# Optimization experiments

Hardware: AMD Instinct MI355X
Metric: run time of the kernel (lower is better)

## Reference

```python
import jax, jax.numpy as jnp
import numpy as np

B, H, W, C, NH, WS = 4, 128, 128, 128, 4, 8
N = WS * WS
HD = C // NH
SCALE = HD ** -0.5
MLP_H = 4 * C


def _rel_index():
    coords = np.stack(np.meshgrid(np.arange(WS), np.arange(WS), indexing='ij'))
    flat = coords.reshape(2, -1)
    rel = (flat[:, :, None] - flat[:, None, :]).transpose(1, 2, 0).astype(np.int64)
    rel[..., 0] += WS - 1
    rel[..., 1] += WS - 1
    rel[..., 0] *= 2 * WS - 1
    return jnp.asarray(rel.sum(-1))  # (N, N)

REL_IDX = _rel_index()


def layer_norm(x, w, b):
    m = jnp.mean(x, -1, keepdims=True)
    v = jnp.mean((x - m) ** 2, -1, keepdims=True)
    return (x - m) * jax.lax.rsqrt(v + 1e-5) * w + b


def window_partition(x):  # (B, H*W, C) -> (B*nW, N, C)
    t = x.reshape(B, H // WS, WS, W // WS, WS, C).transpose(0, 1, 3, 2, 4, 5)
    return t.reshape(-1, N, C)


def window_reverse(wins):  # (B*nW, N, C) -> (B, H*W, C)
    t = wins.reshape(B, H // WS, W // WS, WS, WS, C).transpose(0, 1, 3, 2, 4, 5)
    return t.reshape(B, H * W, C)


def setup_inputs():
    key = jax.random.key(0)
    ks = jax.random.split(key, 8)
    rn = lambda k, s: jax.random.normal(k, s, jnp.float32) * 0.02
    return {
        'x': jax.random.normal(ks[0], (B, H * W, C), jnp.float32),
        'd': jax.random.normal(ks[1], (B, H * W, C), jnp.float32),
        'rpb_table': rn(ks[2], ((2 * WS - 1) ** 2, NH)),
        'norm1_w': jnp.ones((C,), jnp.float32), 'norm1_b': jnp.zeros((C,), jnp.float32),
        'norm2_w': jnp.ones((C,), jnp.float32), 'norm2_b': jnp.zeros((C,), jnp.float32),
        'qkv1_w': rn(ks[3], (4 * C, C)), 'qkv1_b': jnp.zeros((4 * C,), jnp.float32),
        'proj_w': rn(ks[4], (C, C)), 'proj_b': jnp.zeros((C,), jnp.float32),
        'fc1_w': rn(ks[5], (MLP_H, C)), 'fc1_b': jnp.zeros((MLP_H,), jnp.float32),
        'fc2_w': rn(ks[6], (C, MLP_H)), 'fc2_b': jnp.zeros((C,), jnp.float32),
    }


def _attn_core(xw, dw, rpb_table, qkv1_w, qkv1_b, proj_w, proj_b):
    def qkv(t):
        q = (t @ qkv1_w.T + qkv1_b).reshape(-1, N, 4, NH, HD)
        return jnp.moveaxis(q, 2, 0).transpose(0, 1, 3, 2, 4)  # (4, B_, NH, N, HD)

    q_r, k_r, v_r, q_rd = qkv(xw)
    q_d, k_d, v_d, q_dr = qkv(dw)
    bias = rpb_table[REL_IDX].transpose(2, 0, 1)  # (NH, N, N)
    sm = jax.nn.softmax
    dot = lambda q, k: jnp.einsum('bhnd,bhmd->bhnm', q * SCALE, k)
    attn = sm(dot(q_r, k_r) + bias[None])      # bias only on r-branch (as in torch)
    attn_rd = sm(dot(q_dr, k_r))
    attn_d = sm(dot(q_d, k_d))
    attn_dr = sm(dot(q_rd, k_d))
    av = lambda a, v: jnp.einsum('bhnm,bhmd->bhnd', a, v).transpose(0, 2, 1, 3).reshape(-1, N, C)
    x_out = av(attn, v_r) + av(attn_rd, v_r)
    d_out = av(attn_dr, v_d) + av(attn_d, v_d)
    return x_out @ proj_w.T + proj_b, d_out @ proj_w.T + proj_b


def reference(x, d, rpb_table, norm1_w, norm1_b, norm2_w, norm2_b, qkv1_w, qkv1_b, proj_w, proj_b, fc1_w, fc1_b, fc2_w, fc2_b):
    xw = window_partition(layer_norm(x, norm1_w, norm1_b))
    dw = window_partition(layer_norm(d, norm1_w, norm1_b))
    xa, da = _attn_core(xw, dw, rpb_table, qkv1_w, qkv1_b, proj_w, proj_b)
    x = x + window_reverse(xa)
    d = d + window_reverse(da)
    mlp = lambda t: jax.nn.gelu(t @ fc1_w.T + fc1_b, approximate=False) @ fc2_w.T + fc2_b
    x = x + mlp(layer_norm(x, norm2_w, norm2_b))
    d = d + mlp(layer_norm(d, norm2_w, norm2_b))
    return x, d
```

## Files before the change

kernel.cpp:

```cpp
#include <hip/hip_runtime.h>
#include <hip/hip_bf16.h>
#include <math.h>

typedef short bf16x8 __attribute__((ext_vector_type(8)));
typedef float f32x4 __attribute__((ext_vector_type(4)));

#define QKSCALE_L2E 0.25505402227437564f
#define LOG2E 1.4426950408889634f

__device__ __forceinline__ unsigned short f2bf(float f) {
  __hip_bfloat16 h = __float2bfloat16(f);
  return *reinterpret_cast<unsigned short*>(&h);
}
__device__ __forceinline__ float bf2f(unsigned short h) {
  return __uint_as_float(((unsigned int)h) << 16);
}
__device__ __forceinline__ unsigned int pk2(float lo, float hi) {
  __hip_bfloat162 h = __float22bfloat162_rn(make_float2(lo, hi));
  return *reinterpret_cast<unsigned int*>(&h);
}
__device__ __forceinline__ bf16x8 pack8(const float* g) {
  union { unsigned int u[4]; bf16x8 v; } t;
  t.u[0] = pk2(g[0], g[1]); t.u[1] = pk2(g[2], g[3]);
  t.u[2] = pk2(g[4], g[5]); t.u[3] = pk2(g[6], g[7]);
  return t.v;
}

__device__ __forceinline__ bf16x8 ldsv(const unsigned short* base, int row, int strideHalfs, int kHalf, int swzMask) {
  int byte = row * strideHalfs * 2 + kHalf * 2;
  byte ^= (row & swzMask) << 4;
  return *(const bf16x8*)((const char*)base + byte);
}
__device__ __forceinline__ void ldss(unsigned short* base, int row, int strideHalfs, int col, int swzMask, unsigned short v) {
  int byte = row * strideHalfs * 2 + col * 2;
  byte ^= (row & swzMask) << 4;
  *(unsigned short*)((char*)base + byte) = v;
}
__device__ __forceinline__ void ldst64(unsigned short* base, int row, int strideHalfs, int colHalf, int swzMask, unsigned int lo, unsigned int hi) {
  int byte = row * strideHalfs * 2 + colHalf * 2;
  byte ^= (row & swzMask) << 4;
  uint2 val; val.x = lo; val.y = hi;
  *(uint2*)((char*)base + byte) = val;
}
__device__ __forceinline__ void ldst32q(unsigned short* base, int row, int colHalf, unsigned int v) {
  int byte = row * 64 + colHalf * 2;
  byte ^= ((row >> 2) & 1) << 6;
  *(unsigned int*)((char*)base + byte) = v;
}
__device__ __forceinline__ bf16x8 ldsvq(const unsigned short* base, int row, int kHalf) {
  int byte = row * 64 + kHalf * 2;
  byte ^= ((row >> 2) & 1) << 6;
  return *(const bf16x8*)((const char*)base + byte);
}

__global__ void prep_kernel(
    const float* __restrict__ qkv1_w, const float* __restrict__ qkv1_b,
    const float* __restrict__ proj_w, const float* __restrict__ fc1_w,
    const float* __restrict__ fc2_w,  const float* __restrict__ rpb,
    unsigned short* __restrict__ Wqkvf, unsigned short* __restrict__ Wprojf,
    unsigned short* __restrict__ Wfc1f, unsigned short* __restrict__ Wfc2f,
    float* __restrict__ bqkv, float* __restrict__ biasmat)
{
  int i = blockIdx.x * 256 + threadIdx.x;
  if (i < 65536) {
    int j = i & 7, lane = (i >> 3) & 63, kk = (i >> 9) & 3;
    int sub16 = (i >> 11) & 1, h = (i >> 12) & 3, comp = i >> 14;
    int row = comp * 128 + h * 32 + sub16 * 16 + (lane & 15);
    int col = kk * 32 + (lane >> 4) * 8 + j;
    float sc = (comp == 0 || comp == 3) ? QKSCALE_L2E : 1.f;
    Wqkvf[i] = f2bf(qkv1_w[row * 128 + col] * sc);
  }
  int o = i - 65536;
  if (o >= 0 && o < 16384) {
    int j = o & 7, lane = (o >> 3) & 63, kk = (o >> 9) & 3, nf = o >> 11;
    int row = nf * 16 + (lane & 15);
    int cp = kk * 32 + (lane >> 4) * 8 + j;
    int H = cp >> 5, q = cp & 31, a = q >> 1, b = q & 1;
    Wprojf[o] = f2bf(proj_w[row * 128 + H * 32 + 16 * b + a]);
  }
  o -= 16384;
  if (o >= 0 && o < 65536) {
    int j = o & 7, lane = (o >> 3) & 63, kk = (o >> 9) & 3, n16 = o >> 11;
    int row = n16 * 16 + (lane & 15);
    int cp = kk * 32 + (lane >> 4) * 8 + j;
    Wfc1f[o] = f2bf(fc1_w[row * 128 + 16 * (cp & 7) + (cp >> 3)]);
  }
  o -= 65536;
  if (o >= 0 && o < 65536) {
    int j = o & 7, lane = (o >> 3) & 63, kk = (o >> 9) & 15, n8 = o >> 13;
    int row = n8 * 16 + (lane & 15);
    int m = kk * 32 + (lane >> 4) * 8 + j;
    int src = (m >> 6) * 64 + 16 * (m & 3) + ((m >> 2) & 15);
    Wfc2f[o] = f2bf(fc2_w[row * 512 + src]);
  }
  o -= 65536;
  if (o >= 0 && o < 512) {
    int comp = o >> 7;
    bqkv[o] = qkv1_b[o] * ((comp == 0 || comp == 3) ? QKSCALE_L2E : 1.f);
  }
  o -= 512;
  if (o >= 0 && o < 16384) {
    int hh = o >> 12, n = (o >> 6) & 63, m = o & 63;
    int di = (n >> 3) - (m >> 3) + 7, dj = (n & 7) - (m & 7) + 7;
    biasmat[o] = rpb[(di * 15 + dj) * 4 + hh] * LOG2E;
  }
}

__global__ void __launch_bounds__(256) ln1_kernel(
    const float* __restrict__ x_in, const float* __restrict__ d_in_,
    const float* __restrict__ n1w, const float* __restrict__ n1b,
    unsigned short* __restrict__ xg)
{
  const int s = blockIdx.x >> 10;
  const int row0 = (blockIdx.x & 1023) * 64;
  const int t = threadIdx.x >> 2, q4 = threadIdx.x & 3;
  const int grow = row0 + t;
  const int b2 = grow >> 14, rem = grow & 16383;
  const int gy = rem >> 7, gx = rem & 127;
  const int win = b2 * 256 + (gy >> 3) * 16 + (gx >> 3);
  const int tok = (gy & 7) * 8 + (gx & 7);
  const float* src = (s ? d_in_ : x_in) + (size_t)grow * 128 + q4 * 32;
  float v[32];
  float sum = 0.f, ss = 0.f;
#pragma unroll
  for (int i = 0; i < 8; ++i) {
    float4 f = ((const float4*)src)[i];
    v[i * 4 + 0] = f.x; v[i * 4 + 1] = f.y; v[i * 4 + 2] = f.z; v[i * 4 + 3] = f.w;
    sum += f.x + f.y + f.z + f.w;
    ss += f.x * f.x + f.y * f.y + f.z * f.z + f.w * f.w;
  }
  sum += __shfl_xor(sum, 1); sum += __shfl_xor(sum, 2);
  ss  += __shfl_xor(ss, 1);  ss  += __shfl_xor(ss, 2);
  float mean = sum * (1.f / 128.f);
  float var = ss * (1.f / 128.f) - mean * mean;
  float rs = rsqrtf(var + 1e-5f);
  unsigned short* base = xg + ((size_t)(s * 1024 + win)) * 8192
                         + ((tok >> 4) * 4 + q4) * 512 + (tok & 15) * 8;
#pragma unroll
  for (int i = 0; i < 4; ++i) {
    float g[8];
#pragma unroll
    for (int jj = 0; jj < 8; ++jj) {
      int c = q4 * 32 + i * 8 + jj;
      g[jj] = (v[i * 8 + jj] - mean) * rs * n1w[c] + n1b[c];
    }
    *(bf16x8*)(base + i * 128) = pack8(g);
  }
}

__global__ void __launch_bounds__(256, 4) attn_kernel(
    const unsigned short* __restrict__ xg,
    const unsigned short* __restrict__ Wqkvf, const float* __restrict__ bqkv,
    const float* __restrict__ biasmat,
    unsigned short* __restrict__ aout)
{
  __shared__ unsigned short smem[2][10240];

  const int tid = threadIdx.x, wid = tid >> 6, lane = tid & 63;
  const int l4 = lane >> 4, l15 = lane & 15;
  const int win = blockIdx.x & 1023, h = blockIdx.x >> 10;
  const f32x4 fzero = {0.f, 0.f, 0.f, 0.f};

  bf16x8 aF[2][4];
#pragma unroll
  for (int s = 0; s < 2; ++s) {
    const unsigned short* xw = xg + ((size_t)(s * 1024 + win)) * 8192;
#pragma unroll
    for (int kk = 0; kk < 4; ++kk)
      aF[s][kk] = *(const bf16x8*)(xw + (wid * 4 + kk) * 512 + lane * 8);
  }

  {
    f32x4 acc[2][8];
#pragma unroll
    for (int s = 0; s < 2; ++s)
#pragma unroll
      for (int n = 0; n < 8; ++n) acc[s][n] = fzero;
#pragma unroll
    for (int kk = 0; kk < 4; ++kk)
#pragma unroll
      for (int nf = 0; nf < 8; ++nf) {
        const int frag = (((nf >> 1) * 4 + h) * 2 + (nf & 1)) * 4 + kk;
        bf16x8 bb = *(const bf16x8*)(Wqkvf + frag * 512 + lane * 8);
        acc[0][nf] = __builtin_amdgcn_mfma_f32_16x16x32_bf16(aF[0][kk], bb, acc[0][nf], 0, 0, 0);
        acc[1][nf] = __builtin_amdgcn_mfma_f32_16x16x32_bf16(aF[1][kk], bb, acc[1][nf], 0, 0, 0);
      }
    float bv[8];
#pragma unroll
    for (int nf = 0; nf < 8; ++nf) bv[nf] = bqkv[(nf >> 1) * 128 + h * 32 + (nf & 1) * 16 + l15];
#pragma unroll
    for (int s = 0; s < 2; ++s)
#pragma unroll
      for (int r = 0; r < 4; ++r) {
        const int tw = wid * 16 + l4 * 4 + r;
        ldst32q(smem[s] + 0,    tw, 2 * l15, pk2(acc[s][0][r] + bv[0], acc[s][1][r] + bv[1]));
        ldst32q(smem[s] + 4096, tw, 2 * l15, pk2(acc[s][2][r] + bv[2], acc[s][3][r] + bv[3]));
        ldst32q(smem[s] + 2048, tw, 2 * l15, pk2(acc[s][6][r] + bv[6], acc[s][7][r] + bv[7]));
        const int vc = 16 * l4 + 4 * r + wid;
        ldss(smem[s] + 8192, l15,      64, vc, 7, f2bf(acc[s][4][r] + bv[4]));
        ldss(smem[s] + 8192, 16 + l15, 64, vc, 7, f2bf(acc[s][5][r] + bv[5]));
      }
  }
  __syncthreads();

  const int s = wid >> 1, kind = wid & 1;
  bf16x8 aR[4], kR[4];
  {
    const unsigned short* Ab = kind ? (smem[1 - s] + 2048) : (smem[s] + 0);
    const unsigned short* Kb = smem[s] + 4096;
#pragma unroll
    for (int mf = 0; mf < 4; ++mf) aR[mf] = ldsvq(Ab, mf * 16 + l15, l4 * 8);
#pragma unroll
    for (int nf = 0; nf < 4; ++nf) kR[nf] = ldsvq(Kb, nf * 16 + l15, l4 * 8);
  }

  f32x4 sc[4][4];
#pragma unroll
  for (int mf = 0; mf < 4; ++mf)
#pragma unroll
    for (int nf = 0; nf < 4; ++nf) sc[mf][nf] = fzero;
#pragma unroll
  for (int mf = 0; mf < 4; ++mf)
#pragma unroll
    for (int nf = 0; nf < 4; ++nf)
      sc[mf][nf] = __builtin_amdgcn_mfma_f32_16x16x32_bf16(aR[mf], kR[nf], sc[mf][nf], 0, 0, 0);

  if (s == 0 && kind == 0) {
#pragma unroll
    for (int mf = 0; mf < 4; ++mf)
#pragma unroll
      for (int nf = 0; nf < 4; ++nf)
#pragma unroll
        for (int r = 0; r < 4; ++r) {
          int row = mf * 16 + l4 * 4 + r, col = nf * 16 + l15;
          sc[mf][nf][r] += biasmat[(h * 64 + row) * 64 + col];
        }
  }
#pragma unroll
  for (int mf = 0; mf < 4; ++mf) {
    float M = sc[mf][0][0];
#pragma unroll
    for (int nf = 0; nf < 4; ++nf)
#pragma unroll
      for (int r = 0; r < 4; ++r) M = fmaxf(M, sc[mf][nf][r]);
    M = fmaxf(M, __shfl_xor(M, 1));
    M = fmaxf(M, __shfl_xor(M, 2));
    M = fmaxf(M, __shfl_xor(M, 4));
    M = fmaxf(M, __shfl_xor(M, 8));
#pragma unroll
    for (int r = 0; r < 4; ++r) {
      float e0 = __builtin_amdgcn_exp2f(sc[mf][0][r] - M);
      float e1 = __builtin_amdgcn_exp2f(sc[mf][1][r] - M);
      float e2 = __builtin_amdgcn_exp2f(sc[mf][2][r] - M);
      float e3 = __builtin_amdgcn_exp2f(sc[mf][3][r] - M);
      float sm = e0 + e1 + e2 + e3;
      sm += __shfl_xor(sm, 1); sm += __shfl_xor(sm, 2);
      sm += __shfl_xor(sm, 4); sm += __shfl_xor(sm, 8);
      float inv = __builtin_amdgcn_rcpf(sm);
      sc[mf][0][r] = e0 * inv; sc[mf][1][r] = e1 * inv;
      sc[mf][2][r] = e2 * inv; sc[mf][3][r] = e3 * inv;
    }
  }
  __syncthreads();
  {
    unsigned short* Ptgt = smem[s] + (kind ? 4096 : 0);
#pragma unroll
    for (int mf = 0; mf < 4; ++mf)
#pragma unroll
      for (int r = 0; r < 4; ++r)
        ldst64(Ptgt, mf * 16 + l4 * 4 + r, 64, 4 * l15, 7,
               pk2(sc[mf][0][r], sc[mf][1][r]), pk2(sc[mf][2][r], sc[mf][3][r]));
  }
  __syncthreads();

  {
    const unsigned short* Vt = smem[s] + 8192;
    bf16x8 vR[2][2];
#pragma unroll
    for (int kk = 0; kk < 2; ++kk)
#pragma unroll
      for (int nf = 0; nf < 2; ++nf) vR[kk][nf] = ldsv(Vt, nf * 16 + l15, 64, kk * 32 + l4 * 8, 7);
    f32x4 pv[2][2];
    pv[0][0] = fzero; pv[0][1] = fzero; pv[1][0] = fzero; pv[1][1] = fzero;
#pragma unroll
    for (int pb_i = 0; pb_i < 2; ++pb_i) {
      const unsigned short* Pbuf = smem[s] + pb_i * 4096;
#pragma unroll
      for (int kk = 0; kk < 2; ++kk) {
        bf16x8 pa0 = ldsv(Pbuf, kind * 32 + l15, 64, kk * 32 + l4 * 8, 7);
        bf16x8 pa1 = ldsv(Pbuf, kind * 32 + 16 + l15, 64, kk * 32 + l4 * 8, 7);
#pragma unroll
        for (int nf = 0; nf < 2; ++nf) {
          pv[0][nf] = __builtin_amdgcn_mfma_f32_16x16x32_bf16(pa0, vR[kk][nf], pv[0][nf], 0, 0, 0);
          pv[1][nf] = __builtin_amdgcn_mfma_f32_16x16x32_bf16(pa1, vR[kk][nf], pv[1][nf], 0, 0, 0);
        }
      }
    }
#pragma unroll
    for (int mf = 0; mf < 2; ++mf)
#pragma unroll
      for (int r = 0; r < 4; ++r) {
        int tw = kind * 32 + mf * 16 + l4 * 4 + r;
        *(unsigned int*)(aout + ((size_t)s * 65536 + (size_t)win * 64 + tw) * 128 + h * 32 + 2 * l15) =
            pk2(pv[mf][0][r], pv[mf][1][r]);
      }
  }
}

__global__ void __launch_bounds__(256, 4) proj_kernel(
    const unsigned short* __restrict__ aout, const unsigned short* __restrict__ Wprojf,
    const float* __restrict__ projb,
    const float* __restrict__ x_in, const float* __restrict__ d_in_,
    const float* __restrict__ n2w, const float* __restrict__ n2b,
    unsigned short* __restrict__ xv, unsigned short* __restrict__ xn2)
{
  const int tid = threadIdx.x, wid = tid >> 6, lane = tid & 63;
  const int l4 = lane >> 4, l15 = lane & 15;
  const int s = blockIdx.x >> 9, blk = blockIdx.x & 511;
  const int row0 = blk * 128 + wid * 32;
  const unsigned short* A = aout + (size_t)s * 65536 * 128;
  const f32x4 fzero = {0.f, 0.f, 0.f, 0.f};

  bf16x8 aF[2][4];
#pragma unroll
  for (int mf = 0; mf < 2; ++mf)
#pragma unroll
    for (int kk = 0; kk < 4; ++kk)
      aF[mf][kk] = *(const bf16x8*)(A + (size_t)(row0 + mf * 16 + l15) * 128 + kk * 32 + l4 * 8);

  f32x4 acc[2][8];
#pragma unroll
  for (int mf = 0; mf < 2; ++mf)
#pragma unroll
    for (int nf = 0; nf < 8; ++nf) acc[mf][nf] = fzero;
#pragma unroll
  for (int kk = 0; kk < 4; ++kk)
#pragma unroll
    for (int nf = 0; nf < 8; ++nf) {
      bf16x8 bb = *(const bf16x8*)(Wprojf + (nf * 4 + kk) * 512 + lane * 8);
      acc[0][nf] = __builtin_amdgcn_mfma_f32_16x16x32_bf16(aF[0][kk], bb, acc[0][nf], 0, 0, 0);
      acc[1][nf] = __builtin_amdgcn_mfma_f32_16x16x32_bf16(aF[1][kk], bb, acc[1][nf], 0, 0, 0);
    }

  float pbv[8], w2v[8], b2v[8];
#pragma unroll
  for (int nf = 0; nf < 8; ++nf) {
    int col = nf * 16 + l15;
    pbv[nf] = projb[col]; w2v[nf] = n2w[col]; b2v[nf] = n2b[col];
  }
  const float* resid = s ? d_in_ : x_in;
#pragma unroll
  for (int mf = 0; mf < 2; ++mf)
#pragma unroll
    for (int r = 0; r < 4; ++r) {
      int t = row0 + mf * 16 + l4 * 4 + r;
      int w2 = t >> 6, tk = t & 63;
      int b2 = w2 >> 8, hb = (w2 >> 4) & 15, wb = w2 & 15;
      int grow = b2 * 16384 + hb * 1024 + (tk >> 3) * 128 + wb * 8 + (tk & 7);
      float v[8];
      float sum = 0.f, ssq = 0.f;
#pragma unroll
      for (int nf = 0; nf < 8; ++nf) {
        size_t off = (size_t)grow * 128 + nf * 16 + l15;
        float val = acc[mf][nf][r] + pbv[nf] + resid[off];
        v[nf] = val; sum += val; ssq += val * val;
      }
#pragma unroll
      for (int nf = 0; nf < 8; ++nf)
        xv[((size_t)s * 65536 + grow) * 128 + nf * 16 + l15] = f2bf(v[nf]);
      sum += __shfl_xor(sum, 1); sum += __shfl_xor(sum, 2);
      sum += __shfl_xor(sum, 4); sum += __shfl_xor(sum, 8);
      ssq += __shfl_xor(ssq, 1); ssq += __shfl_xor(ssq, 2);
      ssq += __shfl_xor(ssq, 4); ssq += __shfl_xor(ssq, 8);
      float mean = sum * (1.f / 128.f);
      float var = ssq * (1.f / 128.f) - mean * mean;
      float rs = rsqrtf(var + 1e-5f);
      float g[8];
#pragma unroll
      for (int nf = 0; nf < 8; ++nf) g[nf] = (v[nf] - mean) * rs * w2v[nf] + b2v[nf];
      size_t fidx = ((size_t)s * 4096 + (grow >> 4)) * 4 + (l15 >> 2);
      *(bf16x8*)(xn2 + fidx * 512 + ((l15 & 3) * 16 + (grow & 15)) * 8) = pack8(g);
    }
}

__global__ void __launch_bounds__(512, 2) mlp_kernel(
    const unsigned short* __restrict__ xn2, const unsigned short* __restrict__ xv,
    const unsigned short* __restrict__ Wfc1f, const float* __restrict__ fc1b,
    const unsigned short* __restrict__ Wfc2f, const float* __restrict__ fc2b,
    float* __restrict__ out)
{
  __shared__ unsigned short hbuf[32 * 512];
  const int tid = threadIdx.x, wid = tid >> 6, lane = tid & 63;
  const int l4 = lane >> 4, l15 = lane & 15;
  const f32x4 fzero = {0.f, 0.f, 0.f, 0.f};

  bf16x8 wf1[16], wf2[16];
#pragma unroll
  for (int q = 0; q < 16; ++q)
    wf1[q] = *(const bf16x8*)(Wfc1f + (size_t)((wid * 4 + (q >> 2)) * 4 + (q & 3)) * 512 + lane * 8);
#pragma unroll
  for (int kk = 0; kk < 16; ++kk)
    wf2[kk] = *(const bf16x8*)(Wfc2f + (size_t)(wid * 16 + kk) * 512 + lane * 8);

  float b1v[4];
#pragma unroll
  for (int nf = 0; nf < 4; ++nf) b1v[nf] = fc1b[wid * 64 + nf * 16 + l15];
  const float b2c = fc2b[wid * 16 + l15];
  const int ocol = wid * 16 + l15;

  const size_t tokbase = (size_t)blockIdx.x * 256;

  for (int it = 0; it < 8; ++it) {
    if (it) __syncthreads();
    const size_t tb = tokbase + it * 32;
    f32x4 acc[2][4];
#pragma unroll
    for (int mf = 0; mf < 2; ++mf)
#pragma unroll
      for (int nf = 0; nf < 4; ++nf) acc[mf][nf] = fzero;
#pragma unroll
    for (int mf = 0; mf < 2; ++mf)
#pragma unroll
      for (int kk = 0; kk < 4; ++kk) {
        bf16x8 a = *(const bf16x8*)(xn2 + (((tb >> 4) + mf) * 4 + kk) * 512 + lane * 8);
#pragma unroll
        for (int nf = 0; nf < 4; ++nf)
          acc[mf][nf] = __builtin_amdgcn_mfma_f32_16x16x32_bf16(a, wf1[nf * 4 + kk], acc[mf][nf], 0, 0, 0);
      }
#pragma unroll
    for (int mf = 0; mf < 2; ++mf)
#pragma unroll
      for (int r = 0; r < 4; ++r) {
        float g[4];
#pragma unroll
        for (int nf = 0; nf < 4; ++nf) {
          float vv = acc[mf][nf][r] + b1v[nf];
          float x2 = vv * vv;
          float u2 = vv * fmaf(-0.10294455f, x2, -2.3022078f);
          float e = __builtin_amdgcn_exp2f(u2);
          g[nf] = vv * __builtin_amdgcn_rcpf(1.f + e);
        }
        ldst64(hbuf, mf * 16 + l4 * 4 + r, 512, wid * 64 + l15 * 4, 7,
               pk2(g[0], g[1]), pk2(g[2], g[3]));
      }
    __syncthreads();
    f32x4 a2[2];
    a2[0] = fzero; a2[1] = fzero;
#pragma unroll
    for (int kk = 0; kk < 16; ++kk) {
      bf16x8 h0 = ldsv(hbuf, l15, 512, kk * 32 + l4 * 8, 7);
      bf16x8 h1 = ldsv(hbuf, 16 + l15, 512, kk * 32 + l4 * 8, 7);
      a2[0] = __builtin_amdgcn_mfma_f32_16x16x32_bf16(h0, wf2[kk], a2[0], 0, 0, 0);
      a2[1] = __builtin_amdgcn_mfma_f32_16x16x32_bf16(h1, wf2[kk], a2[1], 0, 0, 0);
    }
#pragma unroll
    for (int mf = 0; mf < 2; ++mf)
#pragma unroll
      for (int r = 0; r < 4; ++r) {
        int row = mf * 16 + l4 * 4 + r;
        size_t off = (tb + row) * 128 + ocol;
        float res = bf2f(xv[off]);
        out[off] = a2[mf][r] + b2c + res;
      }
  }
}

extern "C" void kernel_launch(void* const* d_in, const int* in_sizes, int n_in,
                              void* d_out, int out_size, void* d_ws, size_t ws_size,
                              hipStream_t stream) {
  const float* x    = (const float*)d_in[0];
  const float* dd   = (const float*)d_in[1];
  const float* rpb  = (const float*)d_in[2];
  const float* n1w  = (const float*)d_in[3];
  const float* n1b  = (const float*)d_in[4];
  const float* n2w  = (const float*)d_in[5];
  const float* n2b  = (const float*)d_in[6];
  const float* qkvw = (const float*)d_in[7];
  const float* qkvb = (const float*)d_in[8];
  const float* pw   = (const float*)d_in[9];
  const float* pb   = (const float*)d_in[10];
  const float* f1w  = (const float*)d_in[11];
  const float* f1b  = (const float*)d_in[12];
  const float* f2w  = (const float*)d_in[13];
  const float* f2b  = (const float*)d_in[14];
  float* out = (float*)d_out;
  char* ws = (char*)d_ws;
  unsigned short* Wqkvf  = (unsigned short*)(ws);
  unsigned short* Wprojf = (unsigned short*)(ws + 131072);
  unsigned short* Wfc1f  = (unsigned short*)(ws + 163840);
  unsigned short* Wfc2f  = (unsigned short*)(ws + 294912);
  float* bqkv            = (float*)(ws + 425984);
  float* biasmat         = (float*)(ws + 428032);
  unsigned short* aout   = (unsigned short*)(ws + 524288);
  unsigned short* xn2    = (unsigned short*)(ws + 524288 + 33554432);
  unsigned short* xv     = (unsigned short*)(ws + 524288 + 67108864);
  unsigned short* xg     = (unsigned short*)d_out;

  prep_kernel<<<dim3(899), dim3(256), 0, stream>>>(qkvw, qkvb, pw, f1w, f2w, rpb,
                                                   Wqkvf, Wprojf, Wfc1f, Wfc2f, bqkv, biasmat);
  ln1_kernel<<<dim3(2048), dim3(256), 0, stream>>>(x, dd, n1w, n1b, xg);
  attn_kernel<<<dim3(4096), dim3(256), 0, stream>>>(xg, Wqkvf, bqkv, biasmat, aout);
  proj_kernel<<<dim3(1024), dim3(256), 0, stream>>>(aout, Wprojf, pb, x, dd, n2w, n2b, xv, xn2);
  mlp_kernel<<<dim3(512), dim3(512), 0, stream>>>(xn2, xv, Wfc1f, f1b, Wfc2f, f2b, out);
}
```

Baseline: 203.6 us.

## Split attention blocks per stream, recomputing cross-query to halve shared memory

The attention kernel now launches one block per (window, head, stream) instead of one per (window, head) covering both streams. Each block projects Q, K and V for its own stream and recomputes the cross-query projection from the other stream's input. This halves shared memory and per-wave work, so more blocks can be resident (the launch bounds go from 4 to 8). In exchange it adds redundant loads of the other stream's input and redundant weight fetches per block.

```diff
diff --git a/kernel.cpp b/kernel.cpp
--- a/kernel.cpp
+++ b/kernel.cpp
@@ -148,96 +148,94 @@
   }
 }
 
-__global__ void __launch_bounds__(256, 4) attn_kernel(
+__global__ void __launch_bounds__(256, 8) attn_kernel(
     const unsigned short* __restrict__ xg,
     const unsigned short* __restrict__ Wqkvf, const float* __restrict__ bqkv,
     const float* __restrict__ biasmat,
     unsigned short* __restrict__ aout)
 {
-  __shared__ unsigned short smem[2][10240];
+  __shared__ unsigned short smem[10240];
 
   const int tid = threadIdx.x, wid = tid >> 6, lane = tid & 63;
   const int l4 = lane >> 4, l15 = lane & 15;
-  const int win = blockIdx.x & 1023, h = blockIdx.x >> 10;
+  const int win = blockIdx.x & 1023;
+  const int p = blockIdx.x >> 10;
+  const int h = p & 3, s = p >> 2;
   const f32x4 fzero = {0.f, 0.f, 0.f, 0.f};
 
-  bf16x8 aF[2][4];
-#pragma unroll
-  for (int s = 0; s < 2; ++s) {
-    const unsigned short* xw = xg + ((size_t)(s * 1024 + win)) * 8192;
-#pragma unroll
-    for (int kk = 0; kk < 4; ++kk)
-      aF[s][kk] = *(const bf16x8*)(xw + (wid * 4 + kk) * 512 + lane * 8);
-  }
-
+  bf16x8 aFs[4], aFo[4];
   {
-    f32x4 acc[2][8];
-#pragma unroll
-    for (int s = 0; s < 2; ++s)
-#pragma unroll
-      for (int n = 0; n < 8; ++n) acc[s][n] = fzero;
+    const unsigned short* xws = xg + ((size_t)(s * 1024 + win)) * 8192;
+    const unsigned short* xwo = xg + ((size_t)((1 - s) * 1024 + win)) * 8192;
+#pragma unroll
+    for (int kk = 0; kk < 4; ++kk) {
+      aFs[kk] = *(const bf16x8*)(xws + (wid * 4 + kk) * 512 + lane * 8);
+      aFo[kk] = *(const bf16x8*)(xwo + (wid * 4 + kk) * 512 + lane * 8);
+    }
+  }
+
+  {
+    f32x4 acc[8];
+#pragma unroll
+    for (int n = 0; n < 8; ++n) acc[n] = fzero;
 #pragma unroll
     for (int kk = 0; kk < 4; ++kk)
 #pragma unroll
       for (int nf = 0; nf < 8; ++nf) {
         const int frag = (((nf >> 1) * 4 + h) * 2 + (nf & 1)) * 4 + kk;
         bf16x8 bb = *(const bf16x8*)(Wqkvf + frag * 512 + lane * 8);
-        acc[0][nf] = __builtin_amdgcn_mfma_f32_16x16x32_bf16(aF[0][kk], bb, acc[0][nf], 0, 0, 0);
-        acc[1][nf] = __builtin_amdgcn_mfma_f32_16x16x32_bf16(aF[1][kk], bb, acc[1][nf], 0, 0, 0);
+        acc[nf] = __builtin_amdgcn_mfma_f32_16x16x32_bf16(nf < 6 ? aFs[kk] : aFo[kk], bb, acc[nf], 0, 0, 0);
       }
     float bv[8];
 #pragma unroll
     for (int nf = 0; nf < 8; ++nf) bv[nf] = bqkv[(nf >> 1) * 128 + h * 32 + (nf & 1) * 16 + l15];
 #pragma unroll
-    for (int s = 0; s < 2; ++s)
-#pragma unroll
-      for (int r = 0; r < 4; ++r) {
-        const int tw = wid * 16 + l4 * 4 + r;
-        ldst32q(smem[s] + 0,    tw, 2 * l15, pk2(acc[s][0][r] + bv[0], acc[s][1][r] + bv[1]));
-        ldst32q(smem[s] + 4096, tw, 2 * l15, pk2(acc[s][2][r] + bv[2], acc[s][3][r] + bv[3]));
-        ldst32q(smem[s] + 2048, tw, 2 * l15, pk2(acc[s][6][r] + bv[6], acc[s][7][r] + bv[7]));
-        const int vc = 16 * l4 + 4 * r + wid;
-        ldss(smem[s] + 8192, l15,      64, vc, 7, f2bf(acc[s][4][r] + bv[4]));
-        ldss(smem[s] + 8192, 16 + l15, 64, vc, 7, f2bf(acc[s][5][r] + bv[5]));
-      }
+    for (int r = 0; r < 4; ++r) {
+      const int tw = wid * 16 + l4 * 4 + r;
+      ldst32q(smem + 0,    tw, 2 * l15, pk2(acc[0][r] + bv[0], acc[1][r] + bv[1]));
+      ldst32q(smem + 4096, tw, 2 * l15, pk2(acc[2][r] + bv[2], acc[3][r] + bv[3]));
+      ldst32q(smem + 2048, tw, 2 * l15, pk2(acc[6][r] + bv[6], acc[7][r] + bv[7]));
+      const int vc = 16 * l4 + 4 * r + wid;
+      ldss(smem + 8192, l15,      64, vc, 7, f2bf(acc[4][r] + bv[4]));
+      ldss(smem + 8192, 16 + l15, 64, vc, 7, f2bf(acc[5][r] + bv[5]));
+    }
   }
   __syncthreads();
 
-  const int s = wid >> 1, kind = wid & 1;
-  bf16x8 aR[4], kR[4];
+  const int kind = wid & 1, rh = wid >> 1;
+  bf16x8 aR[2], kR[4];
   {
-    const unsigned short* Ab = kind ? (smem[1 - s] + 2048) : (smem[s] + 0);
-    const unsigned short* Kb = smem[s] + 4096;
-#pragma unroll
-    for (int mf = 0; mf < 4; ++mf) aR[mf] = ldsvq(Ab, mf * 16 + l15, l4 * 8);
-#pragma unroll
-    for (int nf = 0; nf < 4; ++nf) kR[nf] = ldsvq(Kb, nf * 16 + l15, l4 * 8);
-  }
-
-  f32x4 sc[4][4];
-#pragma unroll
-  for (int mf = 0; mf < 4; ++mf)
+    const unsigned short* Ab = kind ? (smem + 2048) : (smem + 0);
+#pragma unroll
+    for (int mf = 0; mf < 2; ++mf) aR[mf] = ldsvq(Ab, rh * 32 + mf * 16 + l15, l4 * 8);
+#pragma unroll
+    for (int nf = 0; nf < 4; ++nf) kR[nf] = ldsvq(smem + 4096, nf * 16 + l15, l4 * 8);
+  }
+
+  f32x4 sc[2][4];
+#pragma unroll
+  for (int mf = 0; mf < 2; ++mf)
 #pragma unroll
     for (int nf = 0; nf < 4; ++nf) sc[mf][nf] = fzero;
 #pragma unroll
-  for (int mf = 0; mf < 4; ++mf)
+  for (int mf = 0; mf < 2; ++mf)
 #pragma unroll
     for (int nf = 0; nf < 4; ++nf)
       sc[mf][nf] = __builtin_amdgcn_mfma_f32_16x16x32_bf16(aR[mf], kR[nf], sc[mf][nf], 0, 0, 0);
 
   if (s == 0 && kind == 0) {
 #pragma unroll
-    for (int mf = 0; mf < 4; ++mf)
+    for (int mf = 0; mf < 2; ++mf)
 #pragma unroll
       for (int nf = 0; nf < 4; ++nf)
 #pragma unroll
         for (int r = 0; r < 4; ++r) {
-          int row = mf * 16 + l4 * 4 + r, col = nf * 16 + l15;
+          int row = rh * 32 + mf * 16 + l4 * 4 + r, col = nf * 16 + l15;
           sc[mf][nf][r] += biasmat[(h * 64 + row) * 64 + col];
         }
   }
 #pragma unroll
-  for (int mf = 0; mf < 4; ++mf) {
+  for (int mf = 0; mf < 2; ++mf) {
     float M = sc[mf][0][0];
 #pragma unroll
     for (int nf = 0; nf < 4; ++nf)
@@ -263,47 +261,42 @@
   }
   __syncthreads();
   {
-    unsigned short* Ptgt = smem[s] + (kind ? 4096 : 0);
-#pragma unroll
-    for (int mf = 0; mf < 4; ++mf)
+    unsigned short* Ptgt = smem + (kind ? 4096 : 0);
+#pragma unroll
+    for (int mf = 0; mf < 2; ++mf)
 #pragma unroll
       for (int r = 0; r < 4; ++r)
-        ldst64(Ptgt, mf * 16 + l4 * 4 + r, 64, 4 * l15, 7,
+        ldst64(Ptgt, rh * 32 + mf * 16 + l4 * 4 + r, 64, 4 * l15, 7,
                pk2(sc[mf][0][r], sc[mf][1][r]), pk2(sc[mf][2][r], sc[mf][3][r]));
   }
   __syncthreads();
 
   {
-    const unsigned short* Vt = smem[s] + 8192;
+    const unsigned short* Vt = smem + 8192;
     bf16x8 vR[2][2];
 #pragma unroll
     for (int kk = 0; kk < 2; ++kk)
 #pragma unroll
       for (int nf = 0; nf < 2; ++nf) vR[kk][nf] = ldsv(Vt, nf * 16 + l15, 64, kk * 32 + l4 * 8, 7);
-    f32x4 pv[2][2];
-    pv[0][0] = fzero; pv[0][1] = fzero; pv[1][0] = fzero; pv[1][1] = fzero;
+    f32x4 pv[2];
+    pv[0] = fzero; pv[1] = fzero;
 #pragma unroll
     for (int pb_i = 0; pb_i < 2; ++pb_i) {
-      const unsigned short* Pbuf = smem[s] + pb_i * 4096;
+      const unsigned short* Pbuf = smem + pb_i * 4096;
 #pragma unroll
       for (int kk = 0; kk < 2; ++kk) {
-        bf16x8 pa0 = ldsv(Pbuf, kind * 32 + l15, 64, kk * 32 + l4 * 8, 7);
-        bf16x8 pa1 = ldsv(Pbuf, kind * 32 + 16 + l15, 64, kk * 32 + l4 * 8, 7);
-#pragma unroll
-        for (int nf = 0; nf < 2; ++nf) {
-          pv[0][nf] = __builtin_amdgcn_mfma_f32_16x16x32_bf16(pa0, vR[kk][nf], pv[0][nf], 0, 0, 0);
-          pv[1][nf] = __builtin_amdgcn_mfma_f32_16x16x32_bf16(pa1, vR[kk][nf], pv[1][nf], 0, 0, 0);
-        }
-      }
-    }
-#pragma unroll
-    for (int mf = 0; mf < 2; ++mf)
-#pragma unroll
-      for (int r = 0; r < 4; ++r) {
-        int tw = kind * 32 + mf * 16 + l4 * 4 + r;
-        *(unsigned int*)(aout + ((size_t)s * 65536 + (size_t)win * 64 + tw) * 128 + h * 32 + 2 * l15) =
-            pk2(pv[mf][0][r], pv[mf][1][r]);
-      }
+        bf16x8 pa = ldsv(Pbuf, wid * 16 + l15, 64, kk * 32 + l4 * 8, 7);
+#pragma unroll
+        for (int nf = 0; nf < 2; ++nf)
+          pv[nf] = __builtin_amdgcn_mfma_f32_16x16x32_bf16(pa, vR[kk][nf], pv[nf], 0, 0, 0);
+      }
+    }
+#pragma unroll
+    for (int r = 0; r < 4; ++r) {
+      int tw = wid * 16 + l4 * 4 + r;
+      *(unsigned int*)(aout + ((size_t)s * 65536 + (size_t)win * 64 + tw) * 128 + h * 32 + 2 * l15) =
+          pk2(pv[0][r], pv[1][r]);
+    }
   }
 }
 
@@ -499,7 +492,7 @@
   prep_kernel<<<dim3(899), dim3(256), 0, stream>>>(qkvw, qkvb, pw, f1w, f2w, rpb,
                                                    Wqkvf, Wprojf, Wfc1f, Wfc2f, bqkv, biasmat);
   ln1_kernel<<<dim3(2048), dim3(256), 0, stream>>>(x, dd, n1w, n1b, xg);
-  attn_kernel<<<dim3(4096), dim3(256), 0, stream>>>(xg, Wqkvf, bqkv, biasmat, aout);
+  attn_kernel<<<dim3(8192), dim3(256), 0, stream>>>(xg, Wqkvf, bqkv, biasmat, aout);
   proj_kernel<<<dim3(1024), dim3(256), 0, stream>>>(aout, Wprojf, pb, x, dd, n2w, n2b, xv, xn2);
   mlp_kernel<<<dim3(512), dim3(512), 0, stream>>>(xn2, xv, Wfc1f, f1b, Wfc2f, f2b, out);
 }
```

After: 250.5 us. 1.23x slower.
